# Kernel tuning notes

Measured on AMD Instinct MI355X. Metric: run time of the kernel, lower is better.

## Reference

```python
import jax, jax.numpy as jnp
import numpy as np

EMBED = 1024
HEADS = 16
HEAD_DIM = EMBED // HEADS
B, S = 2, 2048


def setup_inputs() -> dict:
    key = jax.random.key(0)
    k1, k2, k3 = jax.random.split(key, 3)
    scale = 1.0 / np.sqrt(EMBED)
    x = jax.random.normal(k1, (B, S, EMBED), dtype=jnp.float32)
    mask = jnp.ones((B, 1, 1, S), dtype=jnp.int32)
    Wqkv = jax.random.normal(k2, (3 * EMBED, EMBED), dtype=jnp.float32) * scale
    bqkv = jnp.zeros((3 * EMBED,), dtype=jnp.float32)
    Wout = jax.random.normal(k3, (EMBED, EMBED), dtype=jnp.float32) * scale
    bout = jnp.zeros((EMBED,), dtype=jnp.float32)
    return {"x": x, "mask": mask, "Wqkv": Wqkv, "bqkv": bqkv, "Wout": Wout, "bout": bout}


def reference(x, mask, Wqkv, bqkv, Wout, bout):
    Bsz, Sl, E = x.shape
    # fused QKV projection (torch Linear: x @ W.T + b)
    qkv = x @ Wqkv.T + bqkv                      # [B, S, 3E]
    qkv = qkv.reshape(Bsz, Sl, 3, HEADS, HEAD_DIM)
    qkv = jnp.transpose(qkv, (0, 2, 3, 1, 4))    # [B, 3, H, S, D]
    q, k, v = qkv[:, 0], qkv[:, 1], qkv[:, 2]    # each [B, H, S, D]
    scores = jnp.einsum("bhqd,bhkd->bhqk", q, k) / np.sqrt(HEAD_DIM)
    scores = jnp.where(mask == 0, -jnp.inf, scores)  # mask broadcasts [B,1,1,S]
    attn = jax.nn.softmax(scores, axis=-1)       # dropout is identity at eval
    out = jnp.einsum("bhqk,bhkd->bhqd", attn, v) # [B, H, S, D]
    out = jnp.transpose(out, (0, 2, 1, 3)).reshape(Bsz, Sl, E)
    return out @ Wout.T + bout
```

## Files before the change

kernel.cpp:

```cpp
#include <hip/hip_runtime.h>
#include <stdint.h>

typedef unsigned short u16;
typedef __bf16    bf16x8 __attribute__((ext_vector_type(8)));
typedef u16       u16x8  __attribute__((ext_vector_type(8)));
typedef u16       u16x4  __attribute__((ext_vector_type(4)));
typedef float     f32x4  __attribute__((ext_vector_type(4)));
typedef uint32_t  u32x4  __attribute__((ext_vector_type(4)));

#define MFMA16x16x32(a, b, c) __builtin_amdgcn_mfma_f32_16x16x32_bf16((a), (b), (c), 0, 0, 0)

__device__ __forceinline__ u16 f2bf(float f) {
  uint32_t u = __float_as_uint(f);
  u += 0x7FFFu + ((u >> 16) & 1u);
  return (u16)(u >> 16);
}

__device__ __forceinline__ uint32_t pktrunc(float a, float b) {
  return __builtin_amdgcn_perm(__float_as_uint(b), __float_as_uint(a), 0x07060302u);
}

__device__ __forceinline__ bf16x8 ldfrag(const u16* p) {
  return __builtin_bit_cast(bf16x8, *(const u16x8*)p);
}

__device__ __forceinline__ bf16x8 ldfrag2b(const u16* p0, const u16* p1) {
  uint2 a = *(const uint2*)p0;
  uint2 b = *(const uint2*)p1;
  u32x4 t; t[0] = a.x; t[1] = a.y; t[2] = b.x; t[3] = b.y;
  return __builtin_bit_cast(bf16x8, t);
}

__device__ __forceinline__ void gl2lds16(const u16* g, u16* l) {
  __builtin_amdgcn_global_load_lds(
      (__attribute__((address_space(1))) void*)g,
      (__attribute__((address_space(3))) void*)l, 16, 0, 0);
}

__global__ __launch_bounds__(256) void convert3(
    const float* __restrict__ x, const float* __restrict__ wq,
    const float* __restrict__ wo, u16* __restrict__ xb,
    u16* __restrict__ wqb, u16* __restrict__ wob) {
  const int NX = (4096 * 1024) / 8;
  const int NQ = (3072 * 1024) / 8;
  int i = blockIdx.x * 256 + threadIdx.x;
  const float* s;
  u16* d;
  if (i < NX)           { s = x;  d = xb;  }
  else if (i < NX + NQ) { s = wq; d = wqb; i -= NX; }
  else                  { s = wo; d = wob; i -= NX + NQ; }
  f32x4 a = ((const f32x4*)s)[2 * (size_t)i];
  f32x4 b = ((const f32x4*)s)[2 * (size_t)i + 1];
  u16x8 r;
  #pragma unroll
  for (int e = 0; e < 4; ++e) { r[e] = f2bf(a[e]); r[4 + e] = f2bf(b[e]); }
  ((u16x8*)d)[i] = r;
}

__global__ __launch_bounds__(256) void qkv_gemm(
    const u16* __restrict__ A, const u16* __restrict__ Bw,
    const float* __restrict__ bias, u16* __restrict__ Qo,
    u16* __restrict__ Ko, u16* __restrict__ Vo) {
  __shared__ __align__(16) u16 As[2][128 * 64];
  __shared__ __align__(16) u16 Bs[2][128 * 64];

  const int t = threadIdx.x;
  const int lane = t & 63, w = t >> 6;
  const int quad = lane >> 4, col = lane & 15;
  const int wm = w & 1, wn = w >> 1;
  const int m0 = blockIdx.y * 128, n0 = blockIdx.x * 128;

  f32x4 acc[4][4] = {};

  #pragma unroll
  for (int p = 0; p < 4; ++p) {
    int c = t + 256 * p;
    int r = c >> 3, cc = c & 7;
    int so = (cc ^ (r & 7)) * 8;
    gl2lds16(A  + (size_t)(m0 + r) * 1024 + so, &As[0][0] + c * 8);
    gl2lds16(Bw + (size_t)(n0 + r) * 1024 + so, &Bs[0][0] + c * 8);
  }
  __syncthreads();

  for (int kt = 0; kt < 16; ++kt) {
    const u16* Ac = &As[kt & 1][0];
    const u16* Bc = &Bs[kt & 1][0];
    if (kt < 15) {
      const int ko = (kt + 1) * 64;
      u16* An = &As[(kt + 1) & 1][0];
      u16* Bn = &Bs[(kt + 1) & 1][0];
      #pragma unroll
      for (int p = 0; p < 4; ++p) {
        int c = t + 256 * p;
        int r = c >> 3, cc = c & 7;
        int so = ko + ((cc ^ (r & 7)) * 8);
        gl2lds16(A  + (size_t)(m0 + r) * 1024 + so, An + c * 8);
        gl2lds16(Bw + (size_t)(n0 + r) * 1024 + so, Bn + c * 8);
      }
    }

    #pragma unroll
    for (int kk = 0; kk < 2; ++kk) {
      const int e8 = ((kk * 4 + quad) ^ (col & 7)) * 8;
      bf16x8 bfr[4];
      #pragma unroll
      for (int j = 0; j < 4; ++j)
        bfr[j] = ldfrag(Bc + (wn * 64 + j * 16 + col) * 64 + e8);
      #pragma unroll
      for (int i = 0; i < 4; ++i) {
        bf16x8 afr = ldfrag(Ac + (wm * 64 + i * 16 + col) * 64 + e8);
        #pragma unroll
        for (int j = 0; j < 4; ++j)
          acc[i][j] = MFMA16x16x32(bfr[j], afr, acc[i][j]);
      }
    }
    __syncthreads();
  }

  const int nb = n0 + wn * 64;
  const int which = nb >> 10;
  const int h = (nb >> 6) & 15;
  u16* dst = (which == 0) ? Qo : ((which == 1) ? Ko : Vo);
  const float scale = (which == 0) ? 0.125f : 1.0f;

  #pragma unroll
  for (int j = 0; j < 4; ++j) {
    const f32x4 b4 = *(const f32x4*)(bias + nb + j * 16 + quad * 4);
    #pragma unroll
    for (int i = 0; i < 4; ++i) {
      const int m = m0 + wm * 64 + i * 16 + col;
      const int bb = m >> 11, s = m & 2047;
      u16x4 vv;
      #pragma unroll
      for (int r = 0; r < 4; ++r) vv[r] = f2bf((acc[i][j][r] + b4[r]) * scale);
      *(u16x4*)(dst + ((size_t)(bb * 16 + h) * 2048 + s) * 64 + j * 16 + quad * 4) = vv;
    }
  }
}

__global__ __launch_bounds__(256) void transpose64(
    const u16* __restrict__ V, u16* __restrict__ Vt) {
  __shared__ u16 tile[64][72];
  const int t = threadIdx.x;
  const int s0 = blockIdx.x * 64;
  const int bh = blockIdx.y;
  const u16* Vb = V + (size_t)bh * (2048 * 64);
  u16* Vtb = Vt + (size_t)bh * (64 * 2048);
  #pragma unroll
  for (int p = 0; p < 2; ++p) {
    int c = t + 256 * p;
    int r = c >> 3, c8 = (c & 7) * 8;
    u16x8 v = *(const u16x8*)(Vb + (size_t)(s0 + r) * 64 + c8);
    #pragma unroll
    for (int e = 0; e < 8; ++e) tile[r][c8 + e] = v[e];
  }
  __syncthreads();
  #pragma unroll
  for (int p = 0; p < 2; ++p) {
    int c = t + 256 * p;
    int dr = c >> 3, c8 = (c & 7) * 8;
    u16x8 v;
    #pragma unroll
    for (int e = 0; e < 8; ++e) v[e] = tile[c8 + e][dr];
    *(u16x8*)(Vtb + (size_t)dr * 2048 + s0 + c8) = v;
  }
}

__global__ __launch_bounds__(512, 4) void attn(
    const u16* __restrict__ Q, const u16* __restrict__ K,
    const u16* __restrict__ Vt, const int* __restrict__ mask,
    u16* __restrict__ AO) {
  __shared__ __align__(16) u16 Ks[2][128 * 64];
  __shared__ __align__(16) u16 Vs[2][64 * 128];
  __shared__ __align__(16) u16 Ps[8][32 * 32];

  const int t = threadIdx.x;
  const int lane = t & 63, w = t >> 6;
  const int quad = lane >> 4, col = lane & 15;
  const int g = w & 1, u = w >> 1;
  const int bh = blockIdx.x, qb = blockIdx.y;
  const int b = bh >> 4, h = bh & 15;

  const u16* Qh = Q + (size_t)bh * (2048 * 64);
  const u16* Kh = K + (size_t)bh * (2048 * 64);
  const u16* Vh = Vt + (size_t)bh * (64 * 2048);
  const int* mb = mask + b * 2048;

  u16x8 ou;
  #pragma unroll
  for (int e = 0; e < 8; ++e) ou[e] = 0x3F80;
  const bf16x8 ones = __builtin_bit_cast(bf16x8, ou);

  const int qw = qb * 128 + u * 32;
  const int keyg = g * 64;

  bf16x8 aQ[2][2];
  #pragma unroll
  for (int ct = 0; ct < 2; ++ct) {
    #pragma unroll
    for (int kh = 0; kh < 2; ++kh)
      aQ[ct][kh] = ldfrag(Qh + (size_t)(qw + ct * 16 + col) * 64 + kh * 32 + quad * 8);
  }

  f32x4 o[2][4] = {};
  f32x4 lacc[2] = {};
  u16* Pw = &Ps[w][0];

  #pragma unroll
  for (int p = 0; p < 2; ++p) {
    int c = t + 512 * p;
    int kr = c >> 3, kc = c & 7;
    gl2lds16(Kh + (size_t)kr * 64 + ((kc ^ (kr & 7)) * 8), &Ks[0][0] + c * 8);
    int vr = c >> 4, vc = c & 15;
    gl2lds16(Vh + (size_t)vr * 2048 + ((vc ^ (vr & 15)) * 8), &Vs[0][0] + c * 8);
  }
  __syncthreads();

  for (int kb = 0; kb < 16; ++kb) {
    const int key0 = kb * 128;
    const u16* Kc = &Ks[kb & 1][0];
    const u16* Vc = &Vs[kb & 1][0];

    int4 m4[4];
    #pragma unroll
    for (int jj = 0; jj < 4; ++jj)
      m4[jj] = *(const int4*)(mb + key0 + keyg + jj * 16 + quad * 4);
    __builtin_amdgcn_sched_barrier(0);

    if (kb < 15) {
      u16* Kn = &Ks[(kb + 1) & 1][0];
      u16* Vn = &Vs[(kb + 1) & 1][0];
      #pragma unroll
      for (int p = 0; p < 2; ++p) {
        int c = t + 512 * p;
        int kr = c >> 3, kc = c & 7;
        gl2lds16(Kh + (size_t)(key0 + 128 + kr) * 64 + ((kc ^ (kr & 7)) * 8), Kn + c * 8);
        int vr = c >> 4, vc = c & 15;
        gl2lds16(Vh + (size_t)vr * 2048 + key0 + 128 + ((vc ^ (vr & 15)) * 8), Vn + c * 8);
      }
    }

    f32x4 sc[2][4] = {};
    #pragma unroll
    for (int j = 0; j < 4; ++j) {
      #pragma unroll
      for (int kh = 0; kh < 2; ++kh) {
        bf16x8 ak = ldfrag(Kc + (keyg + j * 16 + col) * 64 + (((kh * 4 + quad) ^ (col & 7)) * 8));
        sc[0][j] = MFMA16x16x32(ak, aQ[0][kh], sc[0][j]);
        sc[1][j] = MFMA16x16x32(ak, aQ[1][kh], sc[1][j]);
      }
    }

    uint32_t M[4][2];
    #pragma unroll
    for (int jj = 0; jj < 4; ++jj) {
      M[jj][0] = (m4[jj].x ? 0x0000FFFFu : 0u) | (m4[jj].y ? 0xFFFF0000u : 0u);
      M[jj][1] = (m4[jj].z ? 0x0000FFFFu : 0u) | (m4[jj].w ? 0xFFFF0000u : 0u);
    }

    #pragma unroll
    for (int sp = 0; sp < 2; ++sp) {
      #pragma unroll
      for (int jj = 0; jj < 2; ++jj) {
        const int j = sp * 2 + jj;
        #pragma unroll
        for (int ct = 0; ct < 2; ++ct) {
          uint2 pk;
          pk.x = pktrunc(__expf(sc[ct][j][0]), __expf(sc[ct][j][1])) & M[j][0];
          pk.y = pktrunc(__expf(sc[ct][j][2]), __expf(sc[ct][j][3])) & M[j][1];
          const int q = ct * 16 + col;
          const int s = (jj * 4 + quad) ^ (q & 7);
          *(uint2*)(Pw + q * 32 + s * 4) = pk;
        }
      }

      bf16x8 bP0 = ldfrag2b(Pw + col * 32 + (((quad * 2) ^ (col & 7)) * 4),
                            Pw + col * 32 + (((quad * 2 + 1) ^ (col & 7)) * 4));
      bf16x8 bP1 = ldfrag2b(Pw + (16 + col) * 32 + (((quad * 2) ^ (col & 7)) * 4),
                            Pw + (16 + col) * 32 + (((quad * 2 + 1) ^ (col & 7)) * 4));
      lacc[0] = MFMA16x16x32(ones, bP0, lacc[0]);
      lacc[1] = MFMA16x16x32(ones, bP1, lacc[1]);
      const int win = g * 2 + sp;
      #pragma unroll
      for (int dt = 0; dt < 4; ++dt) {
        bf16x8 av = ldfrag(Vc + (dt * 16 + col) * 128 + (((win * 4 + quad) ^ col) * 8));
        o[0][dt] = MFMA16x16x32(av, bP0, o[0][dt]);
        o[1][dt] = MFMA16x16x32(av, bP1, o[1][dt]);
      }
    }

    __syncthreads();
  }

  float* Ro = (float*)(&Ks[0][0]) + u * 2048 + lane * 32;
  float* Rl = (float*)(&Vs[0][0]) + u * 128 + lane * 2;
  if (g == 1) {
    #pragma unroll
    for (int ct = 0; ct < 2; ++ct)
      #pragma unroll
      for (int dt = 0; dt < 4; ++dt)
        *(f32x4*)(Ro + ((ct * 4 + dt) ^ (lane & 7)) * 4) = o[ct][dt];
    Rl[0] = lacc[0][0]; Rl[1] = lacc[1][0];
  }
  __syncthreads();
  if (g == 0) {
    float rl[2];
    #pragma unroll
    for (int ct = 0; ct < 2; ++ct) {
      #pragma unroll
      for (int dt = 0; dt < 4; ++dt)
        o[ct][dt] += *(const f32x4*)(Ro + ((ct * 4 + dt) ^ (lane & 7)) * 4);
      rl[ct] = 1.0f / (lacc[ct][0] + Rl[ct]);
    }
    #pragma unroll
    for (int ct = 0; ct < 2; ++ct) {
      const int q = qw + ct * 16 + col;
      #pragma unroll
      for (int dt = 0; dt < 4; ++dt) {
        u16x4 v;
        #pragma unroll
        for (int r = 0; r < 4; ++r) v[r] = f2bf(o[ct][dt][r] * rl[ct]);
        *(u16x4*)(AO + (size_t)(b * 2048 + q) * 1024 + h * 64 + dt * 16 + quad * 4) = v;
      }
    }
  }
}

__global__ __launch_bounds__(256) void proj_gemm(
    const u16* __restrict__ A, const u16* __restrict__ Bw,
    const float* __restrict__ bias, float* __restrict__ out) {
  __shared__ __align__(16) u16 As[2][128 * 64];
  __shared__ __align__(16) u16 Bs[2][64 * 64];

  const int t = threadIdx.x;
  const int lane = t & 63, w = t >> 6;
  const int quad = lane >> 4, col = lane & 15;
  const int wm = w & 1, wn = w >> 1;
  const int m0 = blockIdx.y * 128, n0 = blockIdx.x * 64;

  f32x4 acc[4][2] = {};

  #pragma unroll
  for (int p = 0; p < 4; ++p) {
    int c = t + 256 * p;
    int r = c >> 3, cc = c & 7;
    gl2lds16(A + (size_t)(m0 + r) * 1024 + ((cc ^ (r & 7)) * 8), &As[0][0] + c * 8);
  }
  #pragma unroll
  for (int p = 0; p < 2; ++p) {
    int c = t + 256 * p;
    int r = c >> 3, cc = c & 7;
    gl2lds16(Bw + (size_t)(n0 + r) * 1024 + ((cc ^ (r & 7)) * 8), &Bs[0][0] + c * 8);
  }
  __syncthreads();

  for (int kt = 0; kt < 16; ++kt) {
    const u16* Ac = &As[kt & 1][0];
    const u16* Bc = &Bs[kt & 1][0];
    if (kt < 15) {
      const int ko = (kt + 1) * 64;
      u16* An = &As[(kt + 1) & 1][0];
      u16* Bn = &Bs[(kt + 1) & 1][0];
      #pragma unroll
      for (int p = 0; p < 4; ++p) {
        int c = t + 256 * p;
        int r = c >> 3, cc = c & 7;
        gl2lds16(A + (size_t)(m0 + r) * 1024 + ko + ((cc ^ (r & 7)) * 8), An + c * 8);
      }
      #pragma unroll
      for (int p = 0; p < 2; ++p) {
        int c = t + 256 * p;
        int r = c >> 3, cc = c & 7;
        gl2lds16(Bw + (size_t)(n0 + r) * 1024 + ko + ((cc ^ (r & 7)) * 8), Bn + c * 8);
      }
    }

    #pragma unroll
    for (int kk = 0; kk < 2; ++kk) {
      const int e8 = ((kk * 4 + quad) ^ (col & 7)) * 8;
      bf16x8 bfr[2];
      #pragma unroll
      for (int j = 0; j < 2; ++j)
        bfr[j] = ldfrag(Bc + (wn * 32 + j * 16 + col) * 64 + e8);
      #pragma unroll
      for (int i = 0; i < 4; ++i) {
        bf16x8 afr = ldfrag(Ac + (wm * 64 + i * 16 + col) * 64 + e8);
        #pragma unroll
        for (int j = 0; j < 2; ++j)
          acc[i][j] = MFMA16x16x32(bfr[j], afr, acc[i][j]);
      }
    }
    __syncthreads();
  }

  const int nb = n0 + wn * 32;
  #pragma unroll
  for (int j = 0; j < 2; ++j) {
    const f32x4 b4 = *(const f32x4*)(bias + nb + j * 16 + quad * 4);
    #pragma unroll
    for (int i = 0; i < 4; ++i) {
      const int m = m0 + wm * 64 + i * 16 + col;
      f32x4 vv = acc[i][j] + b4;
      *(f32x4*)(out + (size_t)m * 1024 + nb + j * 16 + quad * 4) = vv;
    }
  }
}

extern "C" void kernel_launch(void* const* d_in, const int* in_sizes, int n_in,
                              void* d_out, int out_size, void* d_ws, size_t ws_size,
                              hipStream_t stream) {
  (void)in_sizes; (void)n_in; (void)out_size; (void)ws_size;
  const float* x    = (const float*)d_in[0];
  const int*   mask = (const int*)d_in[1];
  const float* Wqkv = (const float*)d_in[2];
  const float* bqkv = (const float*)d_in[3];
  const float* Wout = (const float*)d_in[4];
  const float* bout = (const float*)d_in[5];
  float* out = (float*)d_out;
  char* ws = (char*)d_ws;

  u16* Xb  = (u16*)(ws);
  u16* Wqb = (u16*)(ws + ((size_t)8  << 20));
  u16* Wob = (u16*)(ws + ((size_t)14 << 20));
  u16* Qb  = (u16*)(ws + ((size_t)16 << 20));
  u16* Kb  = (u16*)(ws + ((size_t)24 << 20));
  u16* Vb  = (u16*)(ws + ((size_t)32 << 20));
  u16* Vtb = (u16*)(ws + ((size_t)40 << 20));
  u16* AO  = Xb;

  convert3<<<dim3(4096), dim3(256), 0, stream>>>(x, Wqkv, Wout, Xb, Wqb, Wob);
  qkv_gemm<<<dim3(24, 32), dim3(256), 0, stream>>>(Xb, Wqb, bqkv, Qb, Kb, Vb);
  transpose64<<<dim3(32, 32), dim3(256), 0, stream>>>(Vb, Vtb);
  attn<<<dim3(32, 16), dim3(512), 0, stream>>>(Qb, Kb, Vtb, mask, AO);
  proj_gemm<<<dim3(16, 32), dim3(256), 0, stream>>>(AO, Wob, bout, out);
}
```

Before: 207.0 us.

## Remap GEMM blocks per XCD, single-buffer QKV LDS, use exp2 softmax

Both GEMMs now use a 1D grid whose block index is remapped so that blocks landing on the same XCD share a narrow range of weight columns, which should improve L2 reuse. The QKV GEMM drops LDS double buffering in favour of a single buffer with two barriers per k-step, which lowers LDS use and may raise occupancy but removes the overlap of loads with MFMA work. Attention folds log2(e) into the Q scale and calls exp2 directly instead of __expf. The P-tile swizzle also changes so rows 8-15 use a different XOR pattern, aimed at LDS bank conflicts.

```diff
diff --git a/kernel.cpp b/kernel.cpp
--- a/kernel.cpp
+++ b/kernel.cpp
@@ -26,7 +26,7 @@
 
 __device__ __forceinline__ bf16x8 ldfrag2b(const u16* p0, const u16* p1) {
   uint2 a = *(const uint2*)p0;
-  uint2 b = *(const uint2*)p1;
+  uint2 b = *(const uint2*)(p1);
   u32x4 t; t[0] = a.x; t[1] = a.y; t[2] = b.x; t[3] = b.y;
   return __builtin_bit_cast(bf16x8, t);
 }
@@ -61,43 +61,32 @@
     const u16* __restrict__ A, const u16* __restrict__ Bw,
     const float* __restrict__ bias, u16* __restrict__ Qo,
     u16* __restrict__ Ko, u16* __restrict__ Vo) {
-  __shared__ __align__(16) u16 As[2][128 * 64];
-  __shared__ __align__(16) u16 Bs[2][128 * 64];
+  __shared__ __align__(16) u16 As[128 * 64];
+  __shared__ __align__(16) u16 Bs[128 * 64];
 
   const int t = threadIdx.x;
   const int lane = t & 63, w = t >> 6;
   const int quad = lane >> 4, col = lane & 15;
   const int wm = w & 1, wn = w >> 1;
-  const int m0 = blockIdx.y * 128, n0 = blockIdx.x * 128;
+  const int l = blockIdx.x;
+  const int xcd = l & 7, kk2 = l >> 3;
+  const int n0 = (xcd * 3 + (kk2 % 3)) * 128;
+  const int m0 = (kk2 / 3) * 128;
 
   f32x4 acc[4][4] = {};
 
-  #pragma unroll
-  for (int p = 0; p < 4; ++p) {
-    int c = t + 256 * p;
-    int r = c >> 3, cc = c & 7;
-    int so = (cc ^ (r & 7)) * 8;
-    gl2lds16(A  + (size_t)(m0 + r) * 1024 + so, &As[0][0] + c * 8);
-    gl2lds16(Bw + (size_t)(n0 + r) * 1024 + so, &Bs[0][0] + c * 8);
-  }
-  __syncthreads();
-
   for (int kt = 0; kt < 16; ++kt) {
-    const u16* Ac = &As[kt & 1][0];
-    const u16* Bc = &Bs[kt & 1][0];
-    if (kt < 15) {
-      const int ko = (kt + 1) * 64;
-      u16* An = &As[(kt + 1) & 1][0];
-      u16* Bn = &Bs[(kt + 1) & 1][0];
-      #pragma unroll
-      for (int p = 0; p < 4; ++p) {
-        int c = t + 256 * p;
-        int r = c >> 3, cc = c & 7;
-        int so = ko + ((cc ^ (r & 7)) * 8);
-        gl2lds16(A  + (size_t)(m0 + r) * 1024 + so, An + c * 8);
-        gl2lds16(Bw + (size_t)(n0 + r) * 1024 + so, Bn + c * 8);
-      }
-    }
+    const int ko = kt * 64;
+    __syncthreads();
+    #pragma unroll
+    for (int p = 0; p < 4; ++p) {
+      int c = t + 256 * p;
+      int r = c >> 3, cc = c & 7;
+      int so = ko + ((cc ^ (r & 7)) * 8);
+      gl2lds16(A  + (size_t)(m0 + r) * 1024 + so, As + c * 8);
+      gl2lds16(Bw + (size_t)(n0 + r) * 1024 + so, Bs + c * 8);
+    }
+    __syncthreads();
 
     #pragma unroll
     for (int kk = 0; kk < 2; ++kk) {
@@ -105,23 +94,22 @@
       bf16x8 bfr[4];
       #pragma unroll
       for (int j = 0; j < 4; ++j)
-        bfr[j] = ldfrag(Bc + (wn * 64 + j * 16 + col) * 64 + e8);
+        bfr[j] = ldfrag(Bs + (wn * 64 + j * 16 + col) * 64 + e8);
       #pragma unroll
       for (int i = 0; i < 4; ++i) {
-        bf16x8 afr = ldfrag(Ac + (wm * 64 + i * 16 + col) * 64 + e8);
+        bf16x8 afr = ldfrag(As + (wm * 64 + i * 16 + col) * 64 + e8);
         #pragma unroll
         for (int j = 0; j < 4; ++j)
           acc[i][j] = MFMA16x16x32(bfr[j], afr, acc[i][j]);
       }
     }
-    __syncthreads();
   }
 
   const int nb = n0 + wn * 64;
   const int which = nb >> 10;
   const int h = (nb >> 6) & 15;
   u16* dst = (which == 0) ? Qo : ((which == 1) ? Ko : Vo);
-  const float scale = (which == 0) ? 0.125f : 1.0f;
+  const float scale = (which == 0) ? 0.125f * 1.44269504088896f : 1.0f;
 
   #pragma unroll
   for (int j = 0; j < 4; ++j) {
@@ -193,6 +181,7 @@
 
   const int qw = qb * 128 + u * 32;
   const int keyg = g * 64;
+  const int psw = (col & 7) ^ ((col >> 3) << 2);
 
   bf16x8 aQ[2][2];
   #pragma unroll
@@ -266,18 +255,18 @@
         #pragma unroll
         for (int ct = 0; ct < 2; ++ct) {
           uint2 pk;
-          pk.x = pktrunc(__expf(sc[ct][j][0]), __expf(sc[ct][j][1])) & M[j][0];
-          pk.y = pktrunc(__expf(sc[ct][j][2]), __expf(sc[ct][j][3])) & M[j][1];
+          pk.x = pktrunc(__builtin_exp2f(sc[ct][j][0]), __builtin_exp2f(sc[ct][j][1])) & M[j][0];
+          pk.y = pktrunc(__builtin_exp2f(sc[ct][j][2]), __builtin_exp2f(sc[ct][j][3])) & M[j][1];
           const int q = ct * 16 + col;
-          const int s = (jj * 4 + quad) ^ (q & 7);
+          const int s = (jj * 4 + quad) ^ psw;
           *(uint2*)(Pw + q * 32 + s * 4) = pk;
         }
       }
 
-      bf16x8 bP0 = ldfrag2b(Pw + col * 32 + (((quad * 2) ^ (col & 7)) * 4),
-                            Pw + col * 32 + (((quad * 2 + 1) ^ (col & 7)) * 4));
-      bf16x8 bP1 = ldfrag2b(Pw + (16 + col) * 32 + (((quad * 2) ^ (col & 7)) * 4),
-                            Pw + (16 + col) * 32 + (((quad * 2 + 1) ^ (col & 7)) * 4));
+      bf16x8 bP0 = ldfrag2b(Pw + col * 32 + (((quad * 2) ^ psw) * 4),
+                            Pw + col * 32 + (((quad * 2 + 1) ^ psw) * 4));
+      bf16x8 bP1 = ldfrag2b(Pw + (16 + col) * 32 + (((quad * 2) ^ psw) * 4),
+                            Pw + (16 + col) * 32 + (((quad * 2 + 1) ^ psw) * 4));
       lacc[0] = MFMA16x16x32(ones, bP0, lacc[0]);
       lacc[1] = MFMA16x16x32(ones, bP1, lacc[1]);
       const int win = g * 2 + sp;
@@ -336,7 +325,10 @@
   const int lane = t & 63, w = t >> 6;
   const int quad = lane >> 4, col = lane & 15;
   const int wm = w & 1, wn = w >> 1;
-  const int m0 = blockIdx.y * 128, n0 = blockIdx.x * 64;
+  const int l = blockIdx.x;
+  const int xcd = l & 7, kk2 = l >> 3;
+  const int n0 = (xcd * 2 + (kk2 & 1)) * 64;
+  const int m0 = (kk2 >> 1) * 128;
 
   f32x4 acc[4][2] = {};
 
@@ -429,8 +421,8 @@
   u16* AO  = Xb;
 
   convert3<<<dim3(4096), dim3(256), 0, stream>>>(x, Wqkv, Wout, Xb, Wqb, Wob);
-  qkv_gemm<<<dim3(24, 32), dim3(256), 0, stream>>>(Xb, Wqb, bqkv, Qb, Kb, Vb);
+  qkv_gemm<<<dim3(768), dim3(256), 0, stream>>>(Xb, Wqb, bqkv, Qb, Kb, Vb);
   transpose64<<<dim3(32, 32), dim3(256), 0, stream>>>(Vb, Vtb);
   attn<<<dim3(32, 16), dim3(512), 0, stream>>>(Qb, Kb, Vtb, mask, AO);
-  proj_gemm<<<dim3(16, 32), dim3(256), 0, stream>>>(AO, Wob, bout, out);
-}
+  proj_gemm<<<dim3(512), dim3(256), 0, stream>>>(AO, Wob, bout, out);
+}
```

New measurement: 203.2 us. Within noise of the previous version (-1.8%).
